# Performance work log

Hardware: AMD Instinct MI355X
Metric: run time of the kernel (lower is better)

## Reference

```python
import jax, jax.numpy as jnp
import numpy as np

B = 4096
D = 256
TEMP = 0.5


def setup_inputs() -> dict:
    key = jax.random.key(0)
    k1, k2 = jax.random.split(key)
    x_i = jax.random.normal(k1, (B, D), dtype=jnp.float32)
    x_j = jax.random.normal(k2, (B, D), dtype=jnp.float32)
    return {"x_i": x_i, "x_j": x_j}


def reference(x_i, x_j):
    b = x_i.shape[0]
    # L2-normalize rows (F.normalize with default eps=1e-12)
    def l2norm(x):
        n = jnp.linalg.norm(x, axis=1, keepdims=True)
        return x / jnp.maximum(n, 1e-12)

    z = jnp.concatenate([l2norm(x_i), l2norm(x_j)], axis=0)  # [2B, D]
    # rows of z are unit-norm, so cosine similarity == dot product
    sim = z @ z.T  # [2B, 2B]

    # positives: diagonals at offsets +B and -B
    idx = jnp.arange(b)
    sim_ij = sim[idx, idx + b]
    sim_ji = sim[idx + b, idx]
    pos = jnp.concatenate([sim_ij, sim_ji], axis=0)  # [2B]

    nom = jnp.exp(pos / TEMP)
    neg_mask = 1.0 - jnp.eye(2 * b, dtype=sim.dtype)
    denom = jnp.sum(neg_mask * jnp.exp(sim / TEMP), axis=1)  # [2B]
    loss = jnp.sum(-jnp.log(nom / denom)) / (2 * b)
    return loss
```

## Files before the change

### kernel.cpp

```cpp
#include <hip/hip_runtime.h>

#define NB   4096
#define ND   256
#define N2B  8192
#define INV_T 2.0f

typedef __attribute__((ext_vector_type(8))) short bf16x8;
typedef __attribute__((ext_vector_type(4))) float f32x4;

__device__ __forceinline__ void gload_lds16(const void* g, void* l) {
  __builtin_amdgcn_global_load_lds(
      (const __attribute__((address_space(1))) void*)g,
      (__attribute__((address_space(3))) void*)l, 16, 0, 0);
}

__device__ __forceinline__ unsigned short f2b(float f) {
  unsigned int u = __float_as_uint(f);
  u = (u + 0x7fffu + ((u >> 16) & 1u)) >> 16;
  return (unsigned short)u;
}
__device__ __forceinline__ float b2f(unsigned short h) {
  return __uint_as_float(((unsigned int)h) << 16);
}

__global__ __launch_bounds__(256) void k_normalize(
    const float* __restrict__ xi, const float* __restrict__ xj,
    unsigned short* __restrict__ Z, float* __restrict__ diagE,
    float* __restrict__ pos, float* __restrict__ lossAcc,
    unsigned int* __restrict__ ticket) {
  __shared__ float sh[2][256];
  if (blockIdx.x == 0 && threadIdx.x == 0) { *lossAcc = 0.0f; *ticket = 0u; }
  int wave = threadIdx.x >> 6, lane = threadIdx.x & 63;
  int r = (int)blockIdx.x * 2 + (wave & 1);
  bool isJ = wave >= 2;
  const float* src = (isJ ? xj : xi) + (size_t)r * ND;
  int zrow = r + (isJ ? NB : 0);

  float4 v = *(const float4*)(src + lane * 4);
  float ss = v.x * v.x + v.y * v.y + v.z * v.z + v.w * v.w;
#pragma unroll
  for (int m = 1; m < 64; m <<= 1) ss += __shfl_xor(ss, m, 64);
  float scale = 1.0f / fmaxf(sqrtf(ss), 1e-12f);
  unsigned short h0 = f2b(v.x * scale), h1 = f2b(v.y * scale);
  unsigned short h2 = f2b(v.z * scale), h3 = f2b(v.w * scale);
  ushort4 st; st.x = h0; st.y = h1; st.z = h2; st.w = h3;
  *(ushort4*)(Z + (size_t)zrow * ND + lane * 4) = st;

  float f0 = b2f(h0), f1 = b2f(h1), f2 = b2f(h2), f3 = b2f(h3);
  float d = f0 * f0 + f1 * f1 + f2 * f2 + f3 * f3;
#pragma unroll
  for (int m = 1; m < 64; m <<= 1) d += __shfl_xor(d, m, 64);
  if (lane == 0) diagE[zrow] = __expf(d * INV_T);

  if (isJ) {
    float* s = sh[wave & 1] + lane * 4;
    s[0] = f0; s[1] = f1; s[2] = f2; s[3] = f3;
  }
  __syncthreads();
  if (!isJ) {
    const float* s = sh[wave] + lane * 4;
    float p = f0 * s[0] + f1 * s[1] + f2 * s[2] + f3 * s[3];
#pragma unroll
    for (int m = 1; m < 64; m <<= 1) p += __shfl_xor(p, m, 64);
    if (lane == 0) pos[r] = p;
  }
}

#define BK 64
__global__ __launch_bounds__(256) void k_gemm_exp(
    const unsigned short* __restrict__ Z, float* __restrict__ R) {
  __shared__ alignas(16) unsigned short As[128 * BK];
  __shared__ alignas(16) unsigned short Bs[128 * BK];

  int tid = threadIdx.x;
  int wave = tid >> 6, lane = tid & 63;

  int k = (int)blockIdx.x;
  int tm = (int)((sqrtf(8.0f * (float)k + 1.0f) - 1.0f) * 0.5f);
  while ((tm + 1) * (tm + 2) / 2 <= k) ++tm;
  while (tm * (tm + 1) / 2 > k) --tm;
  int tn = k - tm * (tm + 1) / 2;

  int warp_m = wave & 1, warp_n = wave >> 1;
  int quad = lane >> 4, c16 = lane & 15;

  f32x4 acc[4][4] = {};

  const unsigned short* Ag = Z + (size_t)tm * 128 * ND;
  const unsigned short* Bg = Z + (size_t)tn * 128 * ND;

  int lr = lane >> 3;
  int cs = lane & 7;

  for (int s = 0; s < 4; ++s) {
    int k0 = s * BK;
#pragma unroll
    for (int call = 0; call < 4; ++call) {
      int r0 = wave * 32 + call * 8;
      int row = r0 + lr;
      int gc = cs ^ (row & 7);
      int goff = row * ND + k0 + gc * 8;
      gload_lds16(Ag + goff, &As[r0 * BK]);
      gload_lds16(Bg + goff, &Bs[r0 * BK]);
    }
    asm volatile("s_waitcnt vmcnt(0)" ::: "memory");
    __syncthreads();

#pragma unroll
    for (int t = 0; t < 2; ++t) {
      bf16x8 af[4], bfr[4];
      int c = t * 4 + quad;
#pragma unroll
      for (int mi = 0; mi < 4; ++mi) {
        int row = warp_m * 64 + mi * 16 + c16;
        af[mi] = *(const bf16x8*)&As[(row * 8 + (c ^ (row & 7))) * 8];
      }
#pragma unroll
      for (int ni = 0; ni < 4; ++ni) {
        int row = warp_n * 64 + ni * 16 + c16;
        bfr[ni] = *(const bf16x8*)&Bs[(row * 8 + (c ^ (row & 7))) * 8];
      }
#pragma unroll
      for (int mi = 0; mi < 4; ++mi)
#pragma unroll
        for (int ni = 0; ni < 4; ++ni)
          acc[mi][ni] = __builtin_amdgcn_mfma_f32_16x16x32_bf16(
              af[mi], bfr[ni], acc[mi][ni], 0, 0, 0);
    }
    __syncthreads();
  }

  bool off = (tm != tn);
  float rs[4][4];
  float cs4[4] = {0.f, 0.f, 0.f, 0.f};
#pragma unroll
  for (int mi = 0; mi < 4; ++mi)
#pragma unroll
    for (int r = 0; r < 4; ++r) rs[mi][r] = 0.0f;
#pragma unroll
  for (int mi = 0; mi < 4; ++mi)
#pragma unroll
    for (int ni = 0; ni < 4; ++ni)
#pragma unroll
      for (int r = 0; r < 4; ++r) {
        float e = __expf(acc[mi][ni][r] * INV_T);
        rs[mi][r] += e;
        cs4[ni] += e;
      }

#pragma unroll
  for (int m = 1; m <= 8; m <<= 1)
#pragma unroll
    for (int mi = 0; mi < 4; ++mi)
#pragma unroll
      for (int r = 0; r < 4; ++r)
        rs[mi][r] += __shfl_xor(rs[mi][r], m, 64);

  int rowbase = tm * 128 + warp_m * 64;
  int rslot = tn * 2 + warp_n;
#pragma unroll
  for (int mi = 0; mi < 4; ++mi)
#pragma unroll
    for (int r = 0; r < 4; ++r)
      if (c16 == mi * 4 + r)
        R[(size_t)(rowbase + mi * 16 + quad * 4 + r) * 128 + rslot] = rs[mi][r];

  if (off) {
#pragma unroll
    for (int m = 16; m <= 32; m <<= 1)
#pragma unroll
      for (int ni = 0; ni < 4; ++ni)
        cs4[ni] += __shfl_xor(cs4[ni], m, 64);
    if (quad == 0) {
      int colbase = tn * 128 + warp_n * 64;
      int cslot = tm * 2 + warp_m;
#pragma unroll
      for (int ni = 0; ni < 4; ++ni)
        R[(size_t)(colbase + ni * 16 + c16) * 128 + cslot] = cs4[ni];
    }
  }
}

__global__ __launch_bounds__(256) void k_final(
    const float* __restrict__ R, const float* __restrict__ diagE,
    const float* __restrict__ pos, float* __restrict__ lossAcc,
    unsigned int* __restrict__ ticket, float* __restrict__ out) {
  __shared__ float red[4];
  int tid = threadIdx.x;
  int wave = tid >> 6, lane = tid & 63;
  int row = (int)blockIdx.x * 64 + (tid >> 2);
  int c0 = (tid & 3) * 32;

  const float* Rr = R + (size_t)row * 128 + c0;
  float s = 0.0f;
#pragma unroll
  for (int i = 0; i < 8; ++i) {
    float4 v = *(const float4*)(Rr + i * 4);
    s += v.x + v.y + v.z + v.w;
  }
  s += __shfl_xor(s, 1, 64);
  s += __shfl_xor(s, 2, 64);
  float term = (__logf(s - diagE[row]) - INV_T * pos[row & (NB - 1)]) * 0.25f;
#pragma unroll
  for (int m = 1; m < 64; m <<= 1) term += __shfl_xor(term, m, 64);
  if (lane == 0) red[wave] = term;
  __syncthreads();
  if (tid == 0) {
    float bs = red[0] + red[1] + red[2] + red[3];
    atomicAdd(lossAcc, bs);
    __threadfence();
    unsigned int old = atomicAdd(ticket, 1u);
    if (old == 127u) {
      float v = atomicAdd(lossAcc, 0.0f);
      out[0] = v * (1.0f / (float)N2B);
    }
  }
}

extern "C" void kernel_launch(void* const* d_in, const int* in_sizes, int n_in,
                              void* d_out, int out_size, void* d_ws,
                              size_t ws_size, hipStream_t stream) {
  const float* xi = (const float*)d_in[0];
  const float* xj = (const float*)d_in[1];
  float* out = (float*)d_out;
  char* ws = (char*)d_ws;
  unsigned short* Z = (unsigned short*)ws;
  float* R = (float*)(ws + (4u << 20));
  float* pos = (float*)(ws + (8u << 20));
  float* diagE = (float*)(ws + (8u << 20) + 65536);
  float* lossAcc = (float*)(ws + (8u << 20) + 131072);
  unsigned int* ticket = (unsigned int*)(ws + (8u << 20) + 131072 + 64);

  k_normalize<<<dim3(NB / 2), dim3(256), 0, stream>>>(xi, xj, Z, diagE, pos,
                                                      lossAcc, ticket);
  k_gemm_exp<<<dim3(64 * 65 / 2), dim3(256), 0, stream>>>(Z, R);
  k_final<<<dim3(128), dim3(256), 0, stream>>>(R, diagE, pos, lossAcc, ticket,
                                               out);
}
```

Baseline: 103.3 us.

## Replace symmetric triangular tiling with row-band kernel keeping A in registers

The GEMM+exp kernel no longer uses symmetric 128x128 triangle tiles that produced both row and column partial sums. Each block now owns a 128-row band, holds its A fragments in registers, and streams 64-row column tiles of Z through LDS over one eighth of the columns, writing 8 partial sums per row. This removes the K-loop LDS staging of A and simplifies the final reduction, but it computes the full matrix instead of half and loses the symmetry saving, roughly doubling MFMA and exp work. It also has only one barrier-separated load/compute phase per tile with no double buffering.

```diff
diff --git a/kernel.cpp b/kernel.cpp
--- a/kernel.cpp
+++ b/kernel.cpp
@@ -66,119 +66,91 @@
   }
 }
 
-#define BK 64
+#define CT 64
 __global__ __launch_bounds__(256) void k_gemm_exp(
     const unsigned short* __restrict__ Z, float* __restrict__ R) {
-  __shared__ alignas(16) unsigned short As[128 * BK];
-  __shared__ alignas(16) unsigned short Bs[128 * BK];
+  __shared__ alignas(16) unsigned short Bs[CT * ND];
 
   int tid = threadIdx.x;
   int wave = tid >> 6, lane = tid & 63;
-
-  int k = (int)blockIdx.x;
-  int tm = (int)((sqrtf(8.0f * (float)k + 1.0f) - 1.0f) * 0.5f);
-  while ((tm + 1) * (tm + 2) / 2 <= k) ++tm;
-  while (tm * (tm + 1) / 2 > k) --tm;
-  int tn = k - tm * (tm + 1) / 2;
-
-  int warp_m = wave & 1, warp_n = wave >> 1;
+  int band = (int)blockIdx.x >> 3;
+  int colq = (int)blockIdx.x & 7;
   int quad = lane >> 4, c16 = lane & 15;
 
-  f32x4 acc[4][4] = {};
-
-  const unsigned short* Ag = Z + (size_t)tm * 128 * ND;
-  const unsigned short* Bg = Z + (size_t)tn * 128 * ND;
-
-  int lr = lane >> 3;
-  int cs = lane & 7;
-
-  for (int s = 0; s < 4; ++s) {
-    int k0 = s * BK;
-#pragma unroll
-    for (int call = 0; call < 4; ++call) {
-      int r0 = wave * 32 + call * 8;
-      int row = r0 + lr;
-      int gc = cs ^ (row & 7);
-      int goff = row * ND + k0 + gc * 8;
-      gload_lds16(Ag + goff, &As[r0 * BK]);
-      gload_lds16(Bg + goff, &Bs[r0 * BK]);
+  bf16x8 afr[2][8];
+  int rowA = band * 128 + wave * 32;
+#pragma unroll
+  for (int rg = 0; rg < 2; ++rg)
+#pragma unroll
+    for (int kk = 0; kk < 8; ++kk)
+      afr[rg][kk] = *(const bf16x8*)(Z + (size_t)(rowA + rg * 16 + c16) * ND +
+                                     kk * 32 + quad * 8);
+
+  float rs[2][4];
+#pragma unroll
+  for (int rg = 0; rg < 2; ++rg)
+#pragma unroll
+    for (int r = 0; r < 4; ++r) rs[rg][r] = 0.0f;
+
+  int lr1 = lane >> 5;
+  int cs = lane & 31;
+
+  for (int ct = 0; ct < 16; ++ct) {
+    int colbase = colq * 1024 + ct * CT;
+    __syncthreads();
+#pragma unroll
+    for (int j = 0; j < 8; ++j) {
+      int r0 = wave * 16 + j * 2;
+      int row = r0 + lr1;
+      int gc = cs ^ (row & 31);
+      gload_lds16(Z + (size_t)(colbase + row) * ND + gc * 8, &Bs[r0 * ND]);
     }
     asm volatile("s_waitcnt vmcnt(0)" ::: "memory");
     __syncthreads();
 
-#pragma unroll
-    for (int t = 0; t < 2; ++t) {
-      bf16x8 af[4], bfr[4];
-      int c = t * 4 + quad;
-#pragma unroll
-      for (int mi = 0; mi < 4; ++mi) {
-        int row = warp_m * 64 + mi * 16 + c16;
-        af[mi] = *(const bf16x8*)&As[(row * 8 + (c ^ (row & 7))) * 8];
+    f32x4 acc[2][4] = {};
+#pragma unroll
+    for (int kk = 0; kk < 8; ++kk) {
+      bf16x8 bfr[4];
+#pragma unroll
+      for (int ni = 0; ni < 4; ++ni) {
+        int row = ni * 16 + c16;
+        int slot = (kk * 4 + quad) ^ (row & 31);
+        bfr[ni] = *(const bf16x8*)&Bs[row * ND + slot * 8];
       }
 #pragma unroll
-      for (int ni = 0; ni < 4; ++ni) {
-        int row = warp_n * 64 + ni * 16 + c16;
-        bfr[ni] = *(const bf16x8*)&Bs[(row * 8 + (c ^ (row & 7))) * 8];
+      for (int rg = 0; rg < 2; ++rg)
+#pragma unroll
+        for (int ni = 0; ni < 4; ++ni)
+          acc[rg][ni] = __builtin_amdgcn_mfma_f32_16x16x32_bf16(
+              afr[rg][kk], bfr[ni], acc[rg][ni], 0, 0, 0);
+    }
+
+#pragma unroll
+    for (int rg = 0; rg < 2; ++rg)
+#pragma unroll
+      for (int ni = 0; ni < 4; ++ni)
+#pragma unroll
+        for (int r = 0; r < 4; ++r)
+          rs[rg][r] += __expf(acc[rg][ni][r] * INV_T);
+  }
+
+#pragma unroll
+  for (int m = 1; m <= 8; m <<= 1)
+#pragma unroll
+    for (int rg = 0; rg < 2; ++rg)
+#pragma unroll
+      for (int r = 0; r < 4; ++r)
+        rs[rg][r] += __shfl_xor(rs[rg][r], m, 64);
+
+#pragma unroll
+  for (int rg = 0; rg < 2; ++rg)
+#pragma unroll
+    for (int r = 0; r < 4; ++r)
+      if (c16 == rg * 4 + r) {
+        int row = rowA + rg * 16 + quad * 4 + r;
+        R[(size_t)row * 8 + colq] = rs[rg][r];
       }
-#pragma unroll
-      for (int mi = 0; mi < 4; ++mi)
-#pragma unroll
-        for (int ni = 0; ni < 4; ++ni)
-          acc[mi][ni] = __builtin_amdgcn_mfma_f32_16x16x32_bf16(
-              af[mi], bfr[ni], acc[mi][ni], 0, 0, 0);
-    }
-    __syncthreads();
-  }
-
-  bool off = (tm != tn);
-  float rs[4][4];
-  float cs4[4] = {0.f, 0.f, 0.f, 0.f};
-#pragma unroll
-  for (int mi = 0; mi < 4; ++mi)
-#pragma unroll
-    for (int r = 0; r < 4; ++r) rs[mi][r] = 0.0f;
-#pragma unroll
-  for (int mi = 0; mi < 4; ++mi)
-#pragma unroll
-    for (int ni = 0; ni < 4; ++ni)
-#pragma unroll
-      for (int r = 0; r < 4; ++r) {
-        float e = __expf(acc[mi][ni][r] * INV_T);
-        rs[mi][r] += e;
-        cs4[ni] += e;
-      }
-
-#pragma unroll
-  for (int m = 1; m <= 8; m <<= 1)
-#pragma unroll
-    for (int mi = 0; mi < 4; ++mi)
-#pragma unroll
-      for (int r = 0; r < 4; ++r)
-        rs[mi][r] += __shfl_xor(rs[mi][r], m, 64);
-
-  int rowbase = tm * 128 + warp_m * 64;
-  int rslot = tn * 2 + warp_n;
-#pragma unroll
-  for (int mi = 0; mi < 4; ++mi)
-#pragma unroll
-    for (int r = 0; r < 4; ++r)
-      if (c16 == mi * 4 + r)
-        R[(size_t)(rowbase + mi * 16 + quad * 4 + r) * 128 + rslot] = rs[mi][r];
-
-  if (off) {
-#pragma unroll
-    for (int m = 16; m <= 32; m <<= 1)
-#pragma unroll
-      for (int ni = 0; ni < 4; ++ni)
-        cs4[ni] += __shfl_xor(cs4[ni], m, 64);
-    if (quad == 0) {
-      int colbase = tn * 128 + warp_n * 64;
-      int cslot = tm * 2 + warp_m;
-#pragma unroll
-      for (int ni = 0; ni < 4; ++ni)
-        R[(size_t)(colbase + ni * 16 + c16) * 128 + cslot] = cs4[ni];
-    }
-  }
 }
 
 __global__ __launch_bounds__(256) void k_final(
@@ -188,19 +160,13 @@
   __shared__ float red[4];
   int tid = threadIdx.x;
   int wave = tid >> 6, lane = tid & 63;
-  int row = (int)blockIdx.x * 64 + (tid >> 2);
-  int c0 = (tid & 3) * 32;
-
-  const float* Rr = R + (size_t)row * 128 + c0;
-  float s = 0.0f;
-#pragma unroll
-  for (int i = 0; i < 8; ++i) {
-    float4 v = *(const float4*)(Rr + i * 4);
-    s += v.x + v.y + v.z + v.w;
-  }
-  s += __shfl_xor(s, 1, 64);
-  s += __shfl_xor(s, 2, 64);
-  float term = (__logf(s - diagE[row]) - INV_T * pos[row & (NB - 1)]) * 0.25f;
+  int row = (int)blockIdx.x * 256 + tid;
+
+  const float* Rr = R + (size_t)row * 8;
+  float4 a = *(const float4*)(Rr);
+  float4 b = *(const float4*)(Rr + 4);
+  float s = (a.x + a.y + a.z + a.w) + (b.x + b.y + b.z + b.w) - diagE[row];
+  float term = __logf(s) - INV_T * pos[row & (NB - 1)];
 #pragma unroll
   for (int m = 1; m < 64; m <<= 1) term += __shfl_xor(term, m, 64);
   if (lane == 0) red[wave] = term;
@@ -210,7 +176,7 @@
     atomicAdd(lossAcc, bs);
     __threadfence();
     unsigned int old = atomicAdd(ticket, 1u);
-    if (old == 127u) {
+    if (old == 31u) {
       float v = atomicAdd(lossAcc, 0.0f);
       out[0] = v * (1.0f / (float)N2B);
     }
@@ -233,7 +199,7 @@
 
   k_normalize<<<dim3(NB / 2), dim3(256), 0, stream>>>(xi, xj, Z, diagE, pos,
                                                       lossAcc, ticket);
-  k_gemm_exp<<<dim3(64 * 65 / 2), dim3(256), 0, stream>>>(Z, R);
-  k_final<<<dim3(128), dim3(256), 0, stream>>>(R, diagE, pos, lossAcc, ticket,
-                                               out);
-}
+  k_gemm_exp<<<dim3(512), dim3(256), 0, stream>>>(Z, R);
+  k_final<<<dim3(32), dim3(256), 0, stream>>>(R, diagE, pos, lossAcc, ticket,
+                                              out);
+}
```

After: 100.2 us. 3.0% less time.
